# Kernel optimization log

Measured on AMD Instinct MI355X. Metric: run time of the kernel, lower is better.

Reference implementation:

```python
import jax, jax.numpy as jnp
import numpy as np

N, F, L, XN, YN = 500000, 8, 16, 8, 4

def setup_inputs() -> dict:
    key = jax.random.key(0)
    k1, k2, k3, k4, k5 = jax.random.split(key, 5)
    inp = jax.random.normal(k1, (N, F), dtype=jnp.float32)
    x = jax.random.normal(k2, (N, XN), dtype=jnp.float32)
    c = jax.random.normal(k3, (F, L), dtype=jnp.float32)
    # widths in [0.5, 1.5) to avoid exp underflow / div-by-tiny
    b = jax.random.uniform(k4, (F, L), dtype=jnp.float32) + 0.5
    w = jax.random.normal(k5, (L, XN, YN), dtype=jnp.float32)
    return {"inp": inp, "x": x, "c": c, "b": b, "w": w}

def reference(inp, x, c, b, w):
    # Gaussian membership: mu[n, f, l] = exp(-(inp[n,f] - c[f,l])^2 / (2 b[f,l]^2))
    d = inp[:, :, None] - c[None, :, :]                      # [N, F, L]
    mu = jnp.exp(-(d * d) / (2.0 * b * b)[None, :, :])       # [N, F, L]
    # Rule firing strength: product over features, + 0.001 (as in torch code)
    firing = jnp.prod(mu, axis=1) + 0.001                    # [N, L]
    # Normalize over rules
    norm = firing / jnp.sum(firing, axis=1, keepdims=True)   # [N, L]
    # Per-rule linear consequents: rule_out[n, l, y] = x[n] @ w[l]
    rule_out = jnp.einsum('nx,lxy->nly', x, w)               # [N, L, YN]
    # Weighted combine over rules
    out = jnp.einsum('nl,nly->ny', norm, rule_out)           # [N, YN]
    # Match torch output layouts: disanceng [L, N], diwuceng [YN, N]
    return (norm.T, out.T)
```

## Files before the change

kernel.cpp:

```cpp
#include <hip/hip_runtime.h>

#define F 8
#define L 16
#define XN 8
#define YN 4
#define BLK 256

typedef float f32x4 __attribute__((ext_vector_type(4)));

__global__ __launch_bounds__(256) void eafnn_kernel(
    const float* __restrict__ inp,
    const float* __restrict__ x,
    const float* __restrict__ c,
    const float* __restrict__ b,
    const float* __restrict__ w,
    float* __restrict__ out,
    int n_total)
{
    __shared__ __attribute__((aligned(16))) float s_A[F * L];
    __shared__ __attribute__((aligned(16))) float s_B[F * L];
    __shared__ __attribute__((aligned(16))) float s_Cp[F * L];
    __shared__ __attribute__((aligned(16))) float s_C0[L];
    __shared__ __attribute__((aligned(16))) float s_norm[L][BLK];
    __shared__ __attribute__((aligned(16))) float s_y[YN][BLK];

    const int tid = threadIdx.x;
    if (tid < F * L) {
        float bb = b[tid], cc = c[tid];
        float k = -1.4426950408889634f / (2.0f * bb * bb);
        s_A[tid] = k;
        s_B[tid] = -2.0f * k * cc;
        s_Cp[tid] = k * cc * cc;
    }
    __syncthreads();
    if (tid < L) {
        float a = 0.0f;
#pragma unroll
        for (int f = 0; f < F; ++f) a += s_Cp[f * L + tid];
        s_C0[tid] = a;
    }
    __syncthreads();

    const size_t base_n = (size_t)blockIdx.x * BLK;
    int n = (int)base_n + tid;
    if (n >= n_total) n = n_total - 1;

    const f32x4* ip = (const f32x4*)(inp + (size_t)n * F);
    f32x4 a0 = ip[0], a1 = ip[1];
    float fi[F] = {a0.x, a0.y, a0.z, a0.w, a1.x, a1.y, a1.z, a1.w};

    const f32x4* xp = (const f32x4*)(x + (size_t)n * XN);
    f32x4 x0 = xp[0], x1 = xp[1];
    float xv[XN] = {x0.x, x0.y, x0.z, x0.w, x1.x, x1.y, x1.z, x1.w};

    float sacc[L];
#pragma unroll
    for (int lq = 0; lq < L / 4; ++lq) {
        f32x4 cq = *(const f32x4*)&s_C0[lq * 4];
        sacc[lq * 4 + 0] = cq.x;
        sacc[lq * 4 + 1] = cq.y;
        sacc[lq * 4 + 2] = cq.z;
        sacc[lq * 4 + 3] = cq.w;
    }

#pragma unroll
    for (int f = 0; f < F; ++f) {
        float v = fi[f];
        float v2 = v * v;
#pragma unroll
        for (int lq = 0; lq < L / 4; ++lq) {
            f32x4 Aq = *(const f32x4*)&s_A[f * L + lq * 4];
            f32x4 Bq = *(const f32x4*)&s_B[f * L + lq * 4];
            sacc[lq * 4 + 0] = fmaf(Aq.x, v2, fmaf(Bq.x, v, sacc[lq * 4 + 0]));
            sacc[lq * 4 + 1] = fmaf(Aq.y, v2, fmaf(Bq.y, v, sacc[lq * 4 + 1]));
            sacc[lq * 4 + 2] = fmaf(Aq.z, v2, fmaf(Bq.z, v, sacc[lq * 4 + 2]));
            sacc[lq * 4 + 3] = fmaf(Aq.w, v2, fmaf(Bq.w, v, sacc[lq * 4 + 3]));
        }
    }

    float tot = 0.0f;
#pragma unroll
    for (int l = 0; l < L; ++l) {
        float fr = __builtin_amdgcn_exp2f(sacc[l]) + 0.001f;
        sacc[l] = fr;
        tot += fr;
    }
    float inv = __builtin_amdgcn_rcpf(tot);
#pragma unroll
    for (int l = 0; l < L; ++l) {
        float nl = sacc[l] * inv;
        sacc[l] = nl;
        s_norm[l][tid] = nl;
    }

    float acc[YN] = {0.f, 0.f, 0.f, 0.f};
#pragma unroll
    for (int l = 0; l < L; ++l) {
        float t0 = 0.f, t1 = 0.f, t2 = 0.f, t3 = 0.f;
#pragma unroll
        for (int i = 0; i < XN; ++i) {
            f32x4 wq = *(const f32x4*)&w[(l * XN + i) * YN];
            float xs = xv[i];
            t0 = fmaf(xs, wq.x, t0);
            t1 = fmaf(xs, wq.y, t1);
            t2 = fmaf(xs, wq.z, t2);
            t3 = fmaf(xs, wq.w, t3);
        }
        float nl = sacc[l];
        acc[0] = fmaf(nl, t0, acc[0]);
        acc[1] = fmaf(nl, t1, acc[1]);
        acc[2] = fmaf(nl, t2, acc[2]);
        acc[3] = fmaf(nl, t3, acc[3]);
    }
#pragma unroll
    for (int y = 0; y < YN; ++y) s_y[y][tid] = acc[y];

    __syncthreads();

    const int ww = tid >> 6, lane = tid & 63;
    const size_t nidx = base_n + (size_t)lane * 4;
    const bool qok = (nidx + 3) < (size_t)n_total;

#pragma unroll
    for (int r = 0; r < 4; ++r) {
        int row = ww * 4 + r;
        f32x4 v = *(const f32x4*)&s_norm[row][lane * 4];
        if (qok)
            __builtin_nontemporal_store(v, (f32x4*)&out[(size_t)row * n_total + nidx]);
    }
    {
        f32x4 v = *(const f32x4*)&s_y[ww][lane * 4];
        float* out_y = out + (size_t)L * n_total;
        if (qok)
            __builtin_nontemporal_store(v, (f32x4*)&out_y[(size_t)ww * n_total + nidx]);
    }
}

extern "C" void kernel_launch(void* const* d_in, const int* in_sizes, int n_in,
                              void* d_out, int out_size, void* d_ws, size_t ws_size,
                              hipStream_t stream) {
    const float* inp = (const float*)d_in[0];
    const float* x   = (const float*)d_in[1];
    const float* c   = (const float*)d_in[2];
    const float* b   = (const float*)d_in[3];
    const float* w   = (const float*)d_in[4];
    float* out = (float*)d_out;

    int n_total = in_sizes[0] / F;
    int grid = (n_total + BLK - 1) / BLK;
    eafnn_kernel<<<grid, BLK, 0, stream>>>(inp, x, c, b, w, out, n_total);
}
```

Measured before the change: 20.58 us.

## Convert to persistent grid-stride kernel with prefetch of next chunk inputs

Launches a capped grid of 512 blocks that loop over 256-row chunks, which amortizes the per-block setup of the Gaussian coefficient tables. Inside the loop, the next chunk's inp and x rows are prefetched into registers while the current chunk is written out. The cost is two block barriers per iteration and extra register pressure from the prefetch buffers. A grid of only 512 blocks on a 256-CU device may also leave occupancy low, so the latency of this memory-bound kernel could end up less well hidden.

```diff
diff --git a/kernel.cpp b/kernel.cpp
--- a/kernel.cpp
+++ b/kernel.cpp
@@ -5,6 +5,7 @@
 #define XN 8
 #define YN 4
 #define BLK 256
+#define CHUNK 256
 
 typedef float f32x4 __attribute__((ext_vector_type(4)));
 
@@ -15,7 +16,7 @@
     const float* __restrict__ b,
     const float* __restrict__ w,
     float* __restrict__ out,
-    int n_total)
+    int n_total, int n_chunks)
 {
     __shared__ __attribute__((aligned(16))) float s_A[F * L];
     __shared__ __attribute__((aligned(16))) float s_B[F * L];
@@ -41,98 +42,116 @@
     }
     __syncthreads();
 
-    const size_t base_n = (size_t)blockIdx.x * BLK;
-    int n = (int)base_n + tid;
-    if (n >= n_total) n = n_total - 1;
+    auto load_inputs = [&](int chunk, float fi[F], float xv[XN]) {
+        int n = chunk * CHUNK + tid;
+        if (n >= n_total) n = n_total - 1;
+        const f32x4* ip = (const f32x4*)(inp + (size_t)n * F);
+        f32x4 a0 = ip[0], a1 = ip[1];
+        fi[0] = a0.x; fi[1] = a0.y; fi[2] = a0.z; fi[3] = a0.w;
+        fi[4] = a1.x; fi[5] = a1.y; fi[6] = a1.z; fi[7] = a1.w;
+        const f32x4* xp = (const f32x4*)(x + (size_t)n * XN);
+        f32x4 x0 = xp[0], x1 = xp[1];
+        xv[0] = x0.x; xv[1] = x0.y; xv[2] = x0.z; xv[3] = x0.w;
+        xv[4] = x1.x; xv[5] = x1.y; xv[6] = x1.z; xv[7] = x1.w;
+    };
 
-    const f32x4* ip = (const f32x4*)(inp + (size_t)n * F);
-    f32x4 a0 = ip[0], a1 = ip[1];
-    float fi[F] = {a0.x, a0.y, a0.z, a0.w, a1.x, a1.y, a1.z, a1.w};
+    const int ww = tid >> 6, lane = tid & 63;
 
-    const f32x4* xp = (const f32x4*)(x + (size_t)n * XN);
-    f32x4 x0 = xp[0], x1 = xp[1];
-    float xv[XN] = {x0.x, x0.y, x0.z, x0.w, x1.x, x1.y, x1.z, x1.w};
+    int chunk = blockIdx.x;
+    float fi[F], xv[XN];
+    load_inputs(chunk, fi, xv);
 
-    float sacc[L];
-#pragma unroll
-    for (int lq = 0; lq < L / 4; ++lq) {
-        f32x4 cq = *(const f32x4*)&s_C0[lq * 4];
-        sacc[lq * 4 + 0] = cq.x;
-        sacc[lq * 4 + 1] = cq.y;
-        sacc[lq * 4 + 2] = cq.z;
-        sacc[lq * 4 + 3] = cq.w;
-    }
-
-#pragma unroll
-    for (int f = 0; f < F; ++f) {
-        float v = fi[f];
-        float v2 = v * v;
+    while (true) {
+        float sacc[L];
 #pragma unroll
         for (int lq = 0; lq < L / 4; ++lq) {
-            f32x4 Aq = *(const f32x4*)&s_A[f * L + lq * 4];
-            f32x4 Bq = *(const f32x4*)&s_B[f * L + lq * 4];
-            sacc[lq * 4 + 0] = fmaf(Aq.x, v2, fmaf(Bq.x, v, sacc[lq * 4 + 0]));
-            sacc[lq * 4 + 1] = fmaf(Aq.y, v2, fmaf(Bq.y, v, sacc[lq * 4 + 1]));
-            sacc[lq * 4 + 2] = fmaf(Aq.z, v2, fmaf(Bq.z, v, sacc[lq * 4 + 2]));
-            sacc[lq * 4 + 3] = fmaf(Aq.w, v2, fmaf(Bq.w, v, sacc[lq * 4 + 3]));
+            f32x4 cq = *(const f32x4*)&s_C0[lq * 4];
+            sacc[lq * 4 + 0] = cq.x;
+            sacc[lq * 4 + 1] = cq.y;
+            sacc[lq * 4 + 2] = cq.z;
+            sacc[lq * 4 + 3] = cq.w;
         }
-    }
+#pragma unroll
+        for (int f = 0; f < F; ++f) {
+            float v = fi[f];
+            float v2 = v * v;
+#pragma unroll
+            for (int lq = 0; lq < L / 4; ++lq) {
+                f32x4 Aq = *(const f32x4*)&s_A[f * L + lq * 4];
+                f32x4 Bq = *(const f32x4*)&s_B[f * L + lq * 4];
+                sacc[lq * 4 + 0] = fmaf(Aq.x, v2, fmaf(Bq.x, v, sacc[lq * 4 + 0]));
+                sacc[lq * 4 + 1] = fmaf(Aq.y, v2, fmaf(Bq.y, v, sacc[lq * 4 + 1]));
+                sacc[lq * 4 + 2] = fmaf(Aq.z, v2, fmaf(Bq.z, v, sacc[lq * 4 + 2]));
+                sacc[lq * 4 + 3] = fmaf(Aq.w, v2, fmaf(Bq.w, v, sacc[lq * 4 + 3]));
+            }
+        }
 
-    float tot = 0.0f;
+        float tot = 0.0f;
 #pragma unroll
-    for (int l = 0; l < L; ++l) {
-        float fr = __builtin_amdgcn_exp2f(sacc[l]) + 0.001f;
-        sacc[l] = fr;
-        tot += fr;
-    }
-    float inv = __builtin_amdgcn_rcpf(tot);
+        for (int l = 0; l < L; ++l) {
+            float fr = __builtin_amdgcn_exp2f(sacc[l]) + 0.001f;
+            sacc[l] = fr;
+            tot += fr;
+        }
+        float inv = __builtin_amdgcn_rcpf(tot);
 #pragma unroll
-    for (int l = 0; l < L; ++l) {
-        float nl = sacc[l] * inv;
-        sacc[l] = nl;
-        s_norm[l][tid] = nl;
-    }
+        for (int l = 0; l < L; ++l) sacc[l] *= inv;
 
-    float acc[YN] = {0.f, 0.f, 0.f, 0.f};
+        float acc[YN] = {0.f, 0.f, 0.f, 0.f};
 #pragma unroll
-    for (int l = 0; l < L; ++l) {
-        float t0 = 0.f, t1 = 0.f, t2 = 0.f, t3 = 0.f;
+        for (int l = 0; l < L; ++l) {
+            float t0 = 0.f, t1 = 0.f, t2 = 0.f, t3 = 0.f;
 #pragma unroll
-        for (int i = 0; i < XN; ++i) {
-            f32x4 wq = *(const f32x4*)&w[(l * XN + i) * YN];
-            float xs = xv[i];
-            t0 = fmaf(xs, wq.x, t0);
-            t1 = fmaf(xs, wq.y, t1);
-            t2 = fmaf(xs, wq.z, t2);
-            t3 = fmaf(xs, wq.w, t3);
+            for (int i = 0; i < XN; ++i) {
+                f32x4 wq = *(const f32x4*)&w[(l * XN + i) * YN];
+                float xs = xv[i];
+                t0 = fmaf(xs, wq.x, t0);
+                t1 = fmaf(xs, wq.y, t1);
+                t2 = fmaf(xs, wq.z, t2);
+                t3 = fmaf(xs, wq.w, t3);
+            }
+            float nl = sacc[l];
+            acc[0] = fmaf(nl, t0, acc[0]);
+            acc[1] = fmaf(nl, t1, acc[1]);
+            acc[2] = fmaf(nl, t2, acc[2]);
+            acc[3] = fmaf(nl, t3, acc[3]);
         }
-        float nl = sacc[l];
-        acc[0] = fmaf(nl, t0, acc[0]);
-        acc[1] = fmaf(nl, t1, acc[1]);
-        acc[2] = fmaf(nl, t2, acc[2]);
-        acc[3] = fmaf(nl, t3, acc[3]);
-    }
+
+        const int next = chunk + (int)gridDim.x;
+        const bool has_next = next < n_chunks;
+        float fi2[F], xv2[XN];
+        if (has_next) load_inputs(next, fi2, xv2);
+
+        __syncthreads();
 #pragma unroll
-    for (int y = 0; y < YN; ++y) s_y[y][tid] = acc[y];
+        for (int l = 0; l < L; ++l) s_norm[l][tid] = sacc[l];
+#pragma unroll
+        for (int y = 0; y < YN; ++y) s_y[y][tid] = acc[y];
+        __syncthreads();
 
-    __syncthreads();
+        const size_t base_n = (size_t)chunk * CHUNK;
+        const size_t nidx = base_n + (size_t)lane * 4;
+        const bool qok = (nidx + 3) < (size_t)n_total;
+#pragma unroll
+        for (int r = 0; r < 4; ++r) {
+            int row = ww * 4 + r;
+            f32x4 v = *(const f32x4*)&s_norm[row][lane * 4];
+            if (qok)
+                __builtin_nontemporal_store(v, (f32x4*)&out[(size_t)row * n_total + nidx]);
+        }
+        {
+            f32x4 v = *(const f32x4*)&s_y[ww][lane * 4];
+            float* out_y = out + (size_t)L * n_total;
+            if (qok)
+                __builtin_nontemporal_store(v, (f32x4*)&out_y[(size_t)ww * n_total + nidx]);
+        }
 
-    const int ww = tid >> 6, lane = tid & 63;
-    const size_t nidx = base_n + (size_t)lane * 4;
-    const bool qok = (nidx + 3) < (size_t)n_total;
-
+        if (!has_next) break;
+        chunk = next;
 #pragma unroll
-    for (int r = 0; r < 4; ++r) {
-        int row = ww * 4 + r;
-        f32x4 v = *(const f32x4*)&s_norm[row][lane * 4];
-        if (qok)
-            __builtin_nontemporal_store(v, (f32x4*)&out[(size_t)row * n_total + nidx]);
-    }
-    {
-        f32x4 v = *(const f32x4*)&s_y[ww][lane * 4];
-        float* out_y = out + (size_t)L * n_total;
-        if (qok)
-            __builtin_nontemporal_store(v, (f32x4*)&out_y[(size_t)ww * n_total + nidx]);
+        for (int i = 0; i < F; ++i) fi[i] = fi2[i];
+#pragma unroll
+        for (int i = 0; i < XN; ++i) xv[i] = xv2[i];
     }
 }
 
@@ -147,6 +166,7 @@
     float* out = (float*)d_out;
 
     int n_total = in_sizes[0] / F;
-    int grid = (n_total + BLK - 1) / BLK;
-    eafnn_kernel<<<grid, BLK, 0, stream>>>(inp, x, c, b, w, out, n_total);
+    int n_chunks = (n_total + CHUNK - 1) / CHUNK;
+    int grid = n_chunks < 512 ? n_chunks : 512;
+    eafnn_kernel<<<grid, BLK, 0, stream>>>(inp, x, c, b, w, out, n_total, n_chunks);
 }
```

New measurement: 46.10 us. 2.24x slower.
